# Performance work log

Measured on AMD Instinct MI355X. Metric: run time of the kernel, lower is better.

## Reference

```python
import jax, jax.numpy as jnp
import numpy as np

B, C, H, W = 8, 256, 64, 64
CQK = C // 8  # 32


def setup_inputs() -> dict:
    key = jax.random.key(0)
    ks = jax.random.split(key, 8)
    s = 0.05
    return {
        "x": jax.random.normal(ks[0], (B, C, H, W), dtype=jnp.float32),
        "wq": jax.random.normal(ks[1], (CQK, C), dtype=jnp.float32) * s,
        "bq": jax.random.normal(ks[2], (CQK,), dtype=jnp.float32) * s,
        "wk": jax.random.normal(ks[3], (CQK, C), dtype=jnp.float32) * s,
        "bk": jax.random.normal(ks[4], (CQK,), dtype=jnp.float32) * s,
        "wv": jax.random.normal(ks[5], (C, C), dtype=jnp.float32) * s,
        "bv": jax.random.normal(ks[6], (C,), dtype=jnp.float32) * s,
        "gamma": jax.random.normal(ks[7], (1,), dtype=jnp.float32),
    }


def reference(x, wq, bq, wk, bk, wv, bv, gamma):
    b, c, h, w = x.shape
    xf = x.reshape(b, c, h * w)  # [B, C, N]
    # conv1d kernel-size-1 == per-token linear over channels
    f = jnp.einsum('oc,bcn->bon', wq, xf) + bq[None, :, None]  # [B, C/8, N]
    g = jnp.einsum('oc,bcn->bon', wk, xf) + bk[None, :, None]  # [B, C/8, N]
    hh = jnp.einsum('oc,bcn->bon', wv, xf) + bv[None, :, None]  # [B, C, N]
    # scores[b, i, j] = sum_o f[b, o, i] * g[b, o, j]; NO 1/sqrt(d) scaling
    scores = jnp.einsum('boi,boj->bij', f, g)  # [B, N, N]
    # softmax over dim=1 (the f/query index axis), as in the original
    beta = jax.nn.softmax(scores, axis=1)
    # o[b, c, j] = gamma * sum_i hh[b, c, i] * beta[b, i, j] + xf
    o = gamma[0] * jnp.einsum('bci,bij->bcj', hh, beta) + xf
    return o.reshape(b, c, h, w)
```

## Files before the change

### kernel.cpp

```cpp
#include <hip/hip_runtime.h>
#include <stdint.h>

#define B_ 8
#define C_ 256
#define N_ 4096
#define LOG2E 1.44269504088896f
#define NSHIFT_L2E (-14.0f * 1.44269504088896f)

typedef _Float16 half8 __attribute__((ext_vector_type(8)));
typedef _Float16 half4 __attribute__((ext_vector_type(4)));
typedef __fp16  fp16x2 __attribute__((ext_vector_type(2)));
typedef float floatx4 __attribute__((ext_vector_type(4)));

__global__ __launch_bounds__(256) void k_wprep(const float* __restrict__ wq, const float* __restrict__ bq,
                                               const float* __restrict__ wk, const float* __restrict__ bk,
                                               const float* __restrict__ wv, const float* __restrict__ bv,
                                               _Float16* __restrict__ Whf, float* __restrict__ Bh) {
    int r = blockIdx.x;
    int t = threadIdx.x;
    const float* src;
    float bias;
    if (r < 32)      { src = wq + r * 256;        bias = bq[r]; }
    else if (r < 64) { src = wk + (r - 32) * 256; bias = bk[r - 32]; }
    else             { src = wv + (r - 64) * 256; bias = bv[r - 64]; }
    Whf[(t >> 3) * 2560 + r * 8 + (t & 7)] = (_Float16)src[t];
    if (t == 0) Bh[r] = bias;
}

__global__ __launch_bounds__(256) void k_proj(const float* __restrict__ x,
                                              const _Float16* __restrict__ Whf,
                                              const float* __restrict__ Bh,
                                              _Float16* __restrict__ Kf,
                                              _Float16* __restrict__ Qf,
                                              _Float16* __restrict__ Vf) {
    __shared__ float xtile[64 * 65];
    __shared__ _Float16 As[64 * 264] __attribute__((aligned(16)));
    int id = blockIdx.x;
    int b  = id & 7;
    int i0 = (id >> 3) * 64;
    int t = threadIdx.x;
    int w = t >> 6, lane = t & 63, col = lane & 15, q = lane >> 4;
    const float* xb = x + (size_t)b * C_ * N_ + i0;
    for (int cc = 0; cc < 4; ++cc) {
        int cr = t >> 4;
        int ip = (t & 15) * 4;
#pragma unroll
        for (int k = 0; k < 4; ++k)
            *(float4*)&xtile[(cr + 16 * k) * 65 + ip] =
                *(const float4*)&xb[(size_t)(cc * 64 + cr + 16 * k) * N_ + ip];
        __syncthreads();
        int i = t & 63, cb2 = (t >> 6) * 16;
        float v[16];
#pragma unroll
        for (int k = 0; k < 16; ++k) v[k] = xtile[(cb2 + k) * 65 + i];
        half8 h0, h1;
#pragma unroll
        for (int k = 0; k < 8; ++k) { h0[k] = (_Float16)v[k]; h1[k] = (_Float16)v[8 + k]; }
        *(half8*)&As[i * 264 + cc * 64 + cb2] = h0;
        *(half8*)&As[i * 264 + cc * 64 + cb2 + 8] = h1;
        __syncthreads();
    }
    floatx4 acc[4][5];
#pragma unroll
    for (int mt = 0; mt < 4; ++mt)
#pragma unroll
        for (int nt = 0; nt < 5; ++nt) acc[mt][nt] = (floatx4){0.f, 0.f, 0.f, 0.f};
    for (int kc = 0; kc < 8; ++kc) {
        half8 a[4], bf[5];
#pragma unroll
        for (int nt = 0; nt < 5; ++nt)
            bf[nt] = *(const half8*)&Whf[(kc * 4 + q) * 2560 + (w * 80 + nt * 16 + col) * 8];
#pragma unroll
        for (int mt = 0; mt < 4; ++mt)
            a[mt] = *(const half8*)&As[(mt * 16 + col) * 264 + kc * 32 + q * 8];
#pragma unroll
        for (int mt = 0; mt < 4; ++mt)
#pragma unroll
            for (int nt = 0; nt < 5; ++nt)
                acc[mt][nt] = __builtin_amdgcn_mfma_f32_16x16x32_f16(a[mt], bf[nt], acc[mt][nt], 0, 0, 0);
    }
#pragma unroll
    for (int nt = 0; nt < 5; ++nt) {
        int n = w * 80 + nt * 16 + col;
        float bias = Bh[n];
        if (n < 32) {
#pragma unroll
            for (int mt = 0; mt < 4; ++mt)
#pragma unroll
                for (int r = 0; r < 4; ++r) {
                    int i = i0 + mt * 16 + q * 4 + r;
                    Kf[((((size_t)b * 128 + (i >> 5)) * 4 + (n >> 3)) * 32 + (i & 31)) * 8 + (n & 7)]
                        = (_Float16)((acc[mt][nt][r] + bias) * LOG2E);
                }
        } else if (n < 64) {
            int n2 = n - 32;
#pragma unroll
            for (int mt = 0; mt < 4; ++mt)
#pragma unroll
                for (int r = 0; r < 4; ++r) {
                    int j = i0 + mt * 16 + q * 4 + r;
                    Qf[((((size_t)b * 128 + (j >> 5)) * 4 + (n2 >> 3)) * 32 + (j & 31)) * 8 + (n2 & 7)]
                        = (_Float16)(acc[mt][nt][r] + bias);
                }
        } else {
            int c = n - 64;
#pragma unroll
            for (int mt = 0; mt < 4; ++mt) {
                int ib = (i0 >> 4) + mt;
                half4 v4;
#pragma unroll
                for (int r = 0; r < 4; ++r) v4[r] = (_Float16)(acc[mt][nt][r] + bias);
                *(half4*)&Vf[(((size_t)b * 256 + ib) * 256 + c) * 16 + q * 4] = v4;
            }
        }
    }
}

#define PS_BUF 8192

#define ATTN_SBLK(AK, WO)                                                         \
    {                                                                             \
        floatx4 s = __builtin_amdgcn_mfma_f32_16x16x32_f16(AK, bq, cns, 0, 0, 0); \
        float p0 = exp2f(s[0]);                                                   \
        float p1 = exp2f(s[1]);                                                   \
        float p2 = exp2f(s[2]);                                                   \
        float p3 = exp2f(s[3]);                                                   \
        lacc += (p0 + p1) + (p2 + p3);                                            \
        union { fp16x2 v; uint32_t u; } plo, phi;                                 \
        plo.v = __builtin_amdgcn_cvt_pkrtz(p0, p1);                               \
        phi.v = __builtin_amdgcn_cvt_pkrtz(p2, p3);                               \
        uint2 pw; pw.x = plo.u; pw.y = phi.u;                                     \
        *(uint2*)&PsF[WO] = pw;                                                   \
    }

#define ATTN_SUB(COND, H, VC, VN, KKA, KKB, ROFF, WOFF)                           \
    {                                                                             \
        if (COND) {                                                               \
            aK0 = *(const half8*)(pK);                                            \
            aK1 = *(const half8*)(pK + 128);                                      \
            pK += 2048;                                                           \
        }                                                                         \
        if ((H) == 0 || (COND)) {                                                 \
            _Pragma("unroll")                                                     \
            for (int ct = 0; ct < 2; ++ct) {                                      \
                VN[ct * 2 + 0] = *(const half8*)(pV0 + ct * 256);                 \
                VN[ct * 2 + 1] = *(const half8*)(pV1 + ct * 256);                 \
            }                                                                     \
            pV0 += 16384; pV1 += 16384;                                           \
        }                                                                         \
        __builtin_amdgcn_s_setprio(1);                                            \
        _Pragma("unroll")                                                         \
        for (int kk = 0; kk < 2; ++kk) {                                          \
            half8 bfr[4];                                                         \
            _Pragma("unroll")                                                     \
            for (int jt = 0; jt < 4; ++jt)                                        \
                bfr[jt] = *(const half8*)&PsF[(ROFF) + jt * 2048 +                \
                    ((kk ? (KKB) : (KKA)) & 1 ? ro1 : ro0) +                      \
                    ((kk ? (KKB) : (KKA)) >> 1) * 64];                            \
            _Pragma("unroll")                                                     \
            for (int ct = 0; ct < 2; ++ct)                                        \
                _Pragma("unroll")                                                 \
                for (int jt = 0; jt < 4; ++jt)                                    \
                    acc[ct][jt] = __builtin_amdgcn_mfma_f32_16x16x32_f16(         \
                        VC[ct * 2 + kk], bfr[jt], acc[ct][jt], 0, 0, 0);          \
        }                                                                         \
        __builtin_amdgcn_s_setprio(0);                                            \
        if (COND) {                                                               \
            ATTN_SBLK(aK0, (WOFF) + wo0 + (H) * 64)                               \
            ATTN_SBLK(aK1, (WOFF) + wo1 + (H) * 64)                               \
        }                                                                         \
    }

#define ATTN_STEP(IT, ROFF, WOFF)                                                 \
    {                                                                             \
        ATTN_SUB((IT) < 31, 0, vA, vB, 0, 1, ROFF, WOFF)                          \
        ATTN_SUB((IT) < 31, 1, vB, vA, 2, 3, ROFF, WOFF)                          \
        asm volatile("s_waitcnt lgkmcnt(0)\n\ts_barrier" ::: "memory");           \
    }

__global__ __launch_bounds__(512, 4) void k_attn(const _Float16* __restrict__ Kf,
                                                 const _Float16* __restrict__ Qf,
                                                 const _Float16* __restrict__ Vf,
                                                 const float* __restrict__ x,
                                                 const float* __restrict__ gptr,
                                                 float* __restrict__ out) {
    __shared__ _Float16 PsF[2 * PS_BUF] __attribute__((aligned(16)));
    __shared__ float Lp[2][64];
    int id = blockIdx.x;
    int b  = id & 7;
    int j0 = (id >> 3) * 64;
    int t = threadIdx.x;
    int w = t >> 6, lane = t & 63, col = lane & 15, q = lane >> 4;
    int jts = w & 3, ihs = w >> 2;
    int cw  = w * 32;
    const _Float16* Kfb = Kf + (size_t)b * 131072;
    const _Float16* Qfb = Qf + (size_t)b * 131072;
    const _Float16* Vfb = Vf + (size_t)b * 1048576;
    const _Float16* pK  = Kfb + ((ihs * 4 + q) * 32 + col) * 8;
    const _Float16* pV0 = Vfb + ((q >> 1) * 256 + cw + col) * 16 + (q & 1) * 8;
    const _Float16* pV1 = pV0 + 8192;
    const int cswz = col & 7;
    const int ro0 = col * 128 + ((q ^ cswz) << 3);
    const int ro1 = ro0 ^ 32;
    const int wo0 = (jts * 16 + col) * 128 + ((((ihs << 2) + (q >> 1)) ^ cswz) << 3) + (q & 1) * 4;
    const int wo1 = wo0 ^ 16;
    const floatx4 cns = {NSHIFT_L2E, NSHIFT_L2E, NSHIFT_L2E, NSHIFT_L2E};
    floatx4 acc[2][4];
#pragma unroll
    for (int ct = 0; ct < 2; ++ct)
#pragma unroll
        for (int jt = 0; jt < 4; ++jt) acc[ct][jt] = (floatx4){0.f, 0.f, 0.f, 0.f};
    float lacc = 0.f;
    half8 vA[4], vB[4], aK0, aK1;
#pragma unroll
    for (int ct = 0; ct < 2; ++ct) {
        vA[ct * 2 + 0] = *(const half8*)(pV0 + ct * 256);
        vA[ct * 2 + 1] = *(const half8*)(pV1 + ct * 256);
    }
    pV0 += 16384; pV1 += 16384;
    int jj = j0 + jts * 16;
    half8 bq = *(const half8*)&Qfb[(((jj >> 5) * 4 + q) * 32 + ((jj & 31) + col)) * 8];
#pragma unroll
    for (int h = 0; h < 2; ++h) {
        aK0 = *(const half8*)(pK);
        aK1 = *(const half8*)(pK + 128);
        pK += 2048;
        ATTN_SBLK(aK0, wo0 + h * 64)
        ATTN_SBLK(aK1, wo1 + h * 64)
    }
    asm volatile("s_waitcnt lgkmcnt(0)\n\ts_barrier" ::: "memory");
    for (int m = 0; m < 16; ++m) {
        int it = m * 2;
        ATTN_STEP(it,     0,      PS_BUF)
        ATTN_STEP(it + 1, PS_BUF, 0)
    }
    lacc += __shfl_xor(lacc, 16, 64);
    lacc += __shfl_xor(lacc, 32, 64);
    if (lane < 16) Lp[ihs][jts * 16 + lane] = lacc;
    __syncthreads();
    float gamma = gptr[0];
    const float* xb = x + (size_t)b * C_ * N_;
    float* ob = out + (size_t)b * C_ * N_;
#pragma unroll
    for (int jt = 0; jt < 4; ++jt) {
        int jl = jt * 16 + col;
        float li = 1.0f / (Lp[0][jl] + Lp[1][jl]);
        int j = j0 + jl;
#pragma unroll
        for (int ct = 0; ct < 2; ++ct)
#pragma unroll
            for (int r = 0; r < 4; ++r) {
                int c = cw + ct * 16 + q * 4 + r;
                size_t off = (size_t)c * N_ + j;
                ob[off] = gamma * acc[ct][jt][r] * li + xb[off];
            }
    }
}

extern "C" void kernel_launch(void* const* d_in, const int* in_sizes, int n_in,
                              void* d_out, int out_size, void* d_ws, size_t ws_size,
                              hipStream_t stream) {
    const float* x  = (const float*)d_in[0];
    const float* wq = (const float*)d_in[1];
    const float* bq = (const float*)d_in[2];
    const float* wk = (const float*)d_in[3];
    const float* bk = (const float*)d_in[4];
    const float* wv = (const float*)d_in[5];
    const float* bv = (const float*)d_in[6];
    const float* gm = (const float*)d_in[7];
    float* out = (float*)d_out;
    char* ws = (char*)d_ws;
    _Float16* Vf  = (_Float16*)ws;
    _Float16* Kf  = (_Float16*)(ws + 16777216);
    _Float16* Qf  = (_Float16*)(ws + 18874368);
    _Float16* Whf = (_Float16*)(ws + 20971520);
    float*    Bh  = (float*)(ws + 21135360);

    k_wprep<<<dim3(320), 256, 0, stream>>>(wq, bq, wk, bk, wv, bv, Whf, Bh);
    k_proj<<<dim3(512), 256, 0, stream>>>(x, Whf, Bh, Kf, Qf, Vf);
    k_attn<<<dim3(512), 512, 0, stream>>>(Kf, Qf, Vf, x, gm, out);
}
```

Before: 190.9 us.

## Restructure attention pipeline into four-slot P buffer ring with K prefetch

Switches the attention main loop from two 8192-element P buffers, each consumed in two halves, to a ring of four 4096-element buffers with one barrier per 64-key step. K fragments are now prefetched one step ahead into alternating register sets, so score computation uses data loaded in the previous step. The scores are written two slots ahead of where they are read, which decouples the softmax-probability writes from the PV MFMA reads. LDS use stays the same, but more K registers are live and the read and write swizzles change, which could cause bank conflicts or extra register pressure.

```diff
diff --git a/kernel.cpp b/kernel.cpp
--- a/kernel.cpp
+++ b/kernel.cpp
@@ -116,7 +116,7 @@
     }
 }
 
-#define PS_BUF 8192
+#define PS_BUF 4096
 
 #define ATTN_SBLK(AK, WO)                                                         \
     {                                                                             \
@@ -133,20 +133,20 @@
         *(uint2*)&PsF[WO] = pw;                                                   \
     }
 
-#define ATTN_SUB(COND, H, VC, VN, KKA, KKB, ROFF, WOFF)                           \
+#define ATTN_STEP(DO_V, DO_K, DO_S, VCUR, VNXT, KC0, KC1, KN0, KN1, RB, WB)       \
     {                                                                             \
-        if (COND) {                                                               \
-            aK0 = *(const half8*)(pK);                                            \
-            aK1 = *(const half8*)(pK + 128);                                      \
-            pK += 2048;                                                           \
-        }                                                                         \
-        if ((H) == 0 || (COND)) {                                                 \
+        if (DO_V) {                                                               \
             _Pragma("unroll")                                                     \
             for (int ct = 0; ct < 2; ++ct) {                                      \
-                VN[ct * 2 + 0] = *(const half8*)(pV0 + ct * 256);                 \
-                VN[ct * 2 + 1] = *(const half8*)(pV1 + ct * 256);                 \
+                VNXT[ct * 2 + 0] = *(const half8*)(pV0 + ct * 256);               \
+                VNXT[ct * 2 + 1] = *(const half8*)(pV1 + ct * 256);               \
             }                                                                     \
             pV0 += 16384; pV1 += 16384;                                           \
+        }                                                                         \
+        if (DO_K) {                                                               \
+            KN0 = *(const half8*)(pK);                                            \
+            KN1 = *(const half8*)(pK + 128);                                      \
+            pK += 2048;                                                           \
         }                                                                         \
         __builtin_amdgcn_s_setprio(1);                                            \
         _Pragma("unroll")                                                         \
@@ -154,27 +154,19 @@
             half8 bfr[4];                                                         \
             _Pragma("unroll")                                                     \
             for (int jt = 0; jt < 4; ++jt)                                        \
-                bfr[jt] = *(const half8*)&PsF[(ROFF) + jt * 2048 +                \
-                    ((kk ? (KKB) : (KKA)) & 1 ? ro1 : ro0) +                      \
-                    ((kk ? (KKB) : (KKA)) >> 1) * 64];                            \
+                bfr[jt] = *(const half8*)&PsF[(RB) + jt * 1024 + (kk ? ro1 : ro0)]; \
             _Pragma("unroll")                                                     \
             for (int ct = 0; ct < 2; ++ct)                                        \
                 _Pragma("unroll")                                                 \
                 for (int jt = 0; jt < 4; ++jt)                                    \
                     acc[ct][jt] = __builtin_amdgcn_mfma_f32_16x16x32_f16(         \
-                        VC[ct * 2 + kk], bfr[jt], acc[ct][jt], 0, 0, 0);          \
+                        VCUR[ct * 2 + kk], bfr[jt], acc[ct][jt], 0, 0, 0);        \
         }                                                                         \
         __builtin_amdgcn_s_setprio(0);                                            \
-        if (COND) {                                                               \
-            ATTN_SBLK(aK0, (WOFF) + wo0 + (H) * 64)                               \
-            ATTN_SBLK(aK1, (WOFF) + wo1 + (H) * 64)                               \
-        }                                                                         \
-    }
-
-#define ATTN_STEP(IT, ROFF, WOFF)                                                 \
-    {                                                                             \
-        ATTN_SUB((IT) < 31, 0, vA, vB, 0, 1, ROFF, WOFF)                          \
-        ATTN_SUB((IT) < 31, 1, vB, vA, 2, 3, ROFF, WOFF)                          \
+        if (DO_S) {                                                               \
+            ATTN_SBLK(KC0, (WB) + wo0)                                            \
+            ATTN_SBLK(KC1, (WB) + wo1)                                            \
+        }                                                                         \
         asm volatile("s_waitcnt lgkmcnt(0)\n\ts_barrier" ::: "memory");           \
     }
 
@@ -184,7 +176,7 @@
                                                  const float* __restrict__ x,
                                                  const float* __restrict__ gptr,
                                                  float* __restrict__ out) {
-    __shared__ _Float16 PsF[2 * PS_BUF] __attribute__((aligned(16)));
+    __shared__ _Float16 PsF[4 * PS_BUF] __attribute__((aligned(16)));
     __shared__ float Lp[2][64];
     int id = blockIdx.x;
     int b  = id & 7;
@@ -200,9 +192,9 @@
     const _Float16* pV0 = Vfb + ((q >> 1) * 256 + cw + col) * 16 + (q & 1) * 8;
     const _Float16* pV1 = pV0 + 8192;
     const int cswz = col & 7;
-    const int ro0 = col * 128 + ((q ^ cswz) << 3);
+    const int ro0 = col * 64 + ((q ^ cswz) << 3);
     const int ro1 = ro0 ^ 32;
-    const int wo0 = (jts * 16 + col) * 128 + ((((ihs << 2) + (q >> 1)) ^ cswz) << 3) + (q & 1) * 4;
+    const int wo0 = (jts * 16 + col) * 64 + (((ihs << 2) ^ (q >> 1) ^ cswz) << 3) + (q & 1) * 4;
     const int wo1 = wo0 ^ 16;
     const floatx4 cns = {NSHIFT_L2E, NSHIFT_L2E, NSHIFT_L2E, NSHIFT_L2E};
     floatx4 acc[2][4];
@@ -211,7 +203,7 @@
 #pragma unroll
         for (int jt = 0; jt < 4; ++jt) acc[ct][jt] = (floatx4){0.f, 0.f, 0.f, 0.f};
     float lacc = 0.f;
-    half8 vA[4], vB[4], aK0, aK1;
+    half8 vA[4], vB[4], kA0, kA1, kB0, kB1;
 #pragma unroll
     for (int ct = 0; ct < 2; ++ct) {
         vA[ct * 2 + 0] = *(const half8*)(pV0 + ct * 256);
@@ -220,20 +212,30 @@
     pV0 += 16384; pV1 += 16384;
     int jj = j0 + jts * 16;
     half8 bq = *(const half8*)&Qfb[(((jj >> 5) * 4 + q) * 32 + ((jj & 31) + col)) * 8];
-#pragma unroll
-    for (int h = 0; h < 2; ++h) {
-        aK0 = *(const half8*)(pK);
-        aK1 = *(const half8*)(pK + 128);
-        pK += 2048;
-        ATTN_SBLK(aK0, wo0 + h * 64)
-        ATTN_SBLK(aK1, wo1 + h * 64)
-    }
+    kA0 = *(const half8*)(pK);
+    kA1 = *(const half8*)(pK + 128);
+    pK += 2048;
+    ATTN_SBLK(kA0, 0 * PS_BUF + wo0)
+    ATTN_SBLK(kA1, 0 * PS_BUF + wo1)
+    kA0 = *(const half8*)(pK);
+    kA1 = *(const half8*)(pK + 128);
+    pK += 2048;
+    ATTN_SBLK(kA0, 1 * PS_BUF + wo0)
+    ATTN_SBLK(kA1, 1 * PS_BUF + wo1)
+    kA0 = *(const half8*)(pK);
+    kA1 = *(const half8*)(pK + 128);
+    pK += 2048;
     asm volatile("s_waitcnt lgkmcnt(0)\n\ts_barrier" ::: "memory");
-    for (int m = 0; m < 16; ++m) {
-        int it = m * 2;
-        ATTN_STEP(it,     0,      PS_BUF)
-        ATTN_STEP(it + 1, PS_BUF, 0)
-    }
+    for (int m = 0; m < 15; ++m) {
+        ATTN_STEP(1, 1, 1, vA, vB, kA0, kA1, kB0, kB1, 0 * PS_BUF, 2 * PS_BUF)
+        ATTN_STEP(1, 1, 1, vB, vA, kB0, kB1, kA0, kA1, 1 * PS_BUF, 3 * PS_BUF)
+        ATTN_STEP(1, 1, 1, vA, vB, kA0, kA1, kB0, kB1, 2 * PS_BUF, 0 * PS_BUF)
+        ATTN_STEP(1, 1, 1, vB, vA, kB0, kB1, kA0, kA1, 3 * PS_BUF, 1 * PS_BUF)
+    }
+    ATTN_STEP(1, 1, 1, vA, vB, kA0, kA1, kB0, kB1, 0 * PS_BUF, 2 * PS_BUF)
+    ATTN_STEP(1, 0, 1, vB, vA, kB0, kB1, kA0, kA1, 1 * PS_BUF, 3 * PS_BUF)
+    ATTN_STEP(1, 0, 0, vA, vB, kA0, kA1, kB0, kB1, 2 * PS_BUF, 0 * PS_BUF)
+    ATTN_STEP(0, 0, 0, vB, vA, kB0, kB1, kA0, kA1, 3 * PS_BUF, 1 * PS_BUF)
     lacc += __shfl_xor(lacc, 16, 64);
     lacc += __shfl_xor(lacc, 32, 64);
     if (lane < 16) Lp[ihs][jts * 16 + lane] = lacc;
```

Result: no change. 190.4 us (-0.3%).
